# Kernel optimization log

Hardware: AMD Instinct MI355X
Metric: run time of the kernel (lower is better)

Reference implementation:

```python
import jax, jax.numpy as jnp
import numpy as np

B, S, D, H, L = 32, 512, 512, 8, 6
NQ, FF, V, C = 8, 2048, 32000, 10
DK = D // H
EPS = 1e-5


def _layernorm(x, g, b):
    mu = jnp.mean(x, axis=-1, keepdims=True)
    var = jnp.mean(jnp.square(x - mu), axis=-1, keepdims=True)
    return (x - mu) * jax.lax.rsqrt(var + EPS) * g + b


def _pos_encoding(seq_len, dim):
    pos = jnp.arange(seq_len, dtype=jnp.float32)[:, None]
    div = jnp.exp(jnp.arange(0, dim, 2, dtype=jnp.float32) * (-jnp.log(10000.0) / dim))
    pe = jnp.zeros((seq_len, dim), dtype=jnp.float32)
    pe = pe.at[:, 0::2].set(jnp.sin(pos * div))
    pe = pe.at[:, 1::2].set(jnp.cos(pos * div))
    return pe


def setup_inputs() -> dict:
    key = jax.random.key(0)
    ks = jax.random.split(key, 16)
    sd = 0.02
    return {
        "x": jax.random.randint(ks[0], (B, S), 0, V),
        "emb": jax.random.normal(ks[1], (V, D), jnp.float32) * sd,
        "ln1_g": jnp.ones((L, D), jnp.float32),
        "ln1_b": jnp.zeros((L, D), jnp.float32),
        "ln2_g": jnp.ones((L, D), jnp.float32),
        "ln2_b": jnp.zeros((L, D), jnp.float32),
        "attn_w": jax.random.normal(ks[2], (L, D, D), jnp.float32) * sd,
        "attn_b": jnp.zeros((L, D), jnp.float32),
        "theta": jax.random.normal(ks[3], (L, NQ), jnp.float32),
        "ffn_w1": jax.random.normal(ks[4], (L, NQ, FF), jnp.float32) * sd,
        "ffn_b1": jnp.zeros((L, FF), jnp.float32),
        "ffn_w2": jax.random.normal(ks[5], (L, FF, D), jnp.float32) * sd,
        "ffn_b2": jnp.zeros((L, D), jnp.float32),
        "clf_w": jax.random.normal(ks[6], (D, C), jnp.float32) * sd,
        "clf_b": jnp.zeros((C,), jnp.float32),
    }


def reference(x, emb, ln1_g, ln1_b, ln2_g, ln2_b, attn_w, attn_b, theta,
              ffn_w1, ffn_b1, ffn_w2, ffn_b2, clf_w, clf_b):
    h = emb[x] + _pos_encoding(S, D)[None]  # [B,S,D]
    scale = 1.0 / jnp.sqrt(jnp.float32(DK))
    for l in range(L):
        # --- MultiHeadAttentionQuantum: q=k=v=reshape(x), no projections ---
        q = h.reshape(B, S, H, DK)
        scores = jnp.einsum('bihd,bjhd->bhij', q, q) * scale
        p = jax.nn.softmax(scores, axis=-1)
        attn = jnp.einsum('bhij,bjhd->bihd', p, q).reshape(B, S, D)
        attn = attn @ attn_w[l] + attn_b[l]
        h = _layernorm(h + attn, ln1_g[l], ln1_b[l])
        # --- FeedForwardQuantum: per-wire RX-encode -> RY(theta) -> <Z> = cos(x)cos(theta) ---
        qout = jnp.cos(h[..., :NQ]) * jnp.cos(theta[l])  # [B,S,NQ]
        f = jax.nn.relu(qout @ ffn_w1[l] + ffn_b1[l]) @ ffn_w2[l] + ffn_b2[l]
        h = _layernorm(h + f, ln2_g[l], ln2_b[l])
    pooled = jnp.mean(h, axis=1)  # [B,D]
    return pooled @ clf_w + clf_b  # [B,C]
```

## Files before the change

### kernel.cpp

```cpp
#include <hip/hip_runtime.h>
#include <hip/hip_bf16.h>
#include <math.h>

#define BB 32
#define SS 512
#define DD 512
#define HH 8
#define DK 64
#define LL 6
#define NQ 8
#define FF 2048
#define CC 10

typedef unsigned int uint;
typedef unsigned short ushort_t;
using bf16x8 = __attribute__((ext_vector_type(8))) short;
using f32x4  = __attribute__((ext_vector_type(4))) float;

#define MFMA(a, b, c) __builtin_amdgcn_mfma_f32_16x16x32_bf16((a), (b), (c), 0, 0, 0)

union U8 { ushort_t u[8]; bf16x8 v; };

__device__ __forceinline__ void gload16(const void* g, void* l) {
    __builtin_amdgcn_global_load_lds((__attribute__((address_space(1))) void*)g,
                                     (__attribute__((address_space(3))) void*)l,
                                     16, 0, 0);
}

__device__ inline ushort_t f2bf(float x) {
    uint u = __float_as_uint(x);
    u += 0x7FFFu + ((u >> 16) & 1u);
    return (ushort_t)(u >> 16);
}
__device__ inline void tsplit(float v, ushort_t& hi, ushort_t& lo) {
    uint u = __float_as_uint(v);
    hi = (ushort_t)(u >> 16);
    lo = f2bf(v - __uint_as_float(u & 0xFFFF0000u));
}
__device__ inline void tsplit_fast(float v, ushort_t& hi, ushort_t& lo) {
    uint u = __float_as_uint(v);
    hi = (ushort_t)(u >> 16);
    float res = v - __uint_as_float(u & 0xFFFF0000u);
    lo = (ushort_t)(__float_as_uint(res) >> 16);
}
__device__ inline uint packsplit(float v) {
    uint u = __float_as_uint(v) & 0xFFFF0000u;
    uint ru = __float_as_uint(v - __uint_as_float(u));
    ru += 0x7FFFu + ((ru >> 16) & 1u);
    return u | (ru >> 16);
}
__device__ inline float unpackf(uint u) {
    return __uint_as_float(u & 0xFFFF0000u) + __uint_as_float(u << 16);
}

__global__ __launch_bounds__(256) void embed_pe(const int* __restrict__ x,
                                                const float* __restrict__ emb,
                                                uint* __restrict__ Hp) {
    int idx = blockIdx.x * 256 + threadIdx.x;
    if (idx >= BB * SS * DD) return;
    int d = idx & (DD - 1);
    int s = (idx >> 9) & (SS - 1);
    int tok = x[idx >> 9];
    int i2 = d >> 1;
    float freq = expf((float)(2 * i2) * (-9.210340371976184f / (float)DD));
    float ang = (float)s * freq;
    float pe = (d & 1) ? cosf(ang) : sinf(ang);
    Hp[idx] = packsplit(emb[(size_t)tok * DD + d] + pe);
}

__global__ __launch_bounds__(256) void transpose_split_w(const float* __restrict__ in,
                                                         ushort_t* __restrict__ outh,
                                                         ushort_t* __restrict__ outl,
                                                         int K, int N) {
    __shared__ ushort_t th[64][68], tl[64][68];
    int nb = N >> 6;
    int k0 = ((int)blockIdx.x / nb) << 6;
    int n0 = ((int)blockIdx.x % nb) << 6;
    int t = threadIdx.x;
    int r = t >> 2, cb = (t & 3) << 4;
#pragma unroll
    for (int c = 0; c < 4; c++) {
        float4 v = *reinterpret_cast<const float4*>(&in[(size_t)(k0 + r) * N + n0 + cb + 4 * c]);
        float vv[4] = {v.x, v.y, v.z, v.w};
#pragma unroll
        for (int e = 0; e < 4; e++) {
            ushort_t hb, lb; tsplit(vv[e], hb, lb);
            th[r][cb + 4 * c + e] = hb;
            tl[r][cb + 4 * c + e] = lb;
        }
    }
    __syncthreads();
    int n = t >> 2, kb = (t & 3) << 4;
#pragma unroll
    for (int c = 0; c < 4; c++) {
        ushort4 oh, ol;
        oh.x = th[kb + 4 * c + 0][n]; ol.x = tl[kb + 4 * c + 0][n];
        oh.y = th[kb + 4 * c + 1][n]; ol.y = tl[kb + 4 * c + 1][n];
        oh.z = th[kb + 4 * c + 2][n]; ol.z = tl[kb + 4 * c + 2][n];
        oh.w = th[kb + 4 * c + 3][n]; ol.w = tl[kb + 4 * c + 3][n];
        *reinterpret_cast<ushort4*>(&outh[(size_t)(n0 + n) * K + k0 + kb + 4 * c]) = oh;
        *reinterpret_cast<ushort4*>(&outl[(size_t)(n0 + n) * K + k0 + kb + 4 * c]) = ol;
    }
}

__global__ __launch_bounds__(256) void prep_w1t(const float* __restrict__ W1all,
                                                ushort_t* __restrict__ outh,
                                                ushort_t* __restrict__ outl) {
    int l = blockIdx.y;
    int f = blockIdx.x * 256 + threadIdx.x;
    const float* W1 = W1all + (size_t)l * NQ * FF;
    U8 ph, pl;
#pragma unroll
    for (int n = 0; n < 8; n++) {
        ushort_t hb, lb; tsplit(W1[n * FF + f], hb, lb);
        ph.u[n] = hb; pl.u[n] = lb;
    }
    *reinterpret_cast<bf16x8*>(&outh[((size_t)l * FF + f) * 8]) = ph.v;
    *reinterpret_cast<bf16x8*>(&outl[((size_t)l * FF + f) * 8]) = pl.v;
}

__global__ __launch_bounds__(512, 4) void flash_attn_split(const uint* __restrict__ Hp,
                                                           ushort_t* __restrict__ outh,
                                                           ushort_t* __restrict__ outl) {
    __shared__ __align__(16) ushort_t Kh[64][72], Kl[64][72];
    __shared__ __align__(16) ushort_t Vh[64][72], Vl[64][72];
    __shared__ __align__(16) ushort_t Ph[128][72], Pl[128][72];

    int i0 = blockIdx.x * 128;
    int h0 = blockIdx.y * DK;
    int b  = blockIdx.z;
    const uint* baseH = Hp + (size_t)b * (SS * DD);

    int t = threadIdx.x;
    int w = t >> 6;
    int ln = t & 63;
    int l15 = ln & 15, lh = ln >> 4;

    bf16x8 aqh0, aqh1, aql0, aql1;
    {
        int row = i0 + w * 16 + l15;
        const uint* src = &baseH[(size_t)row * DD + h0 + lh * 8];
        uint4 p0 = *reinterpret_cast<const uint4*>(src);
        uint4 p1 = *reinterpret_cast<const uint4*>(src + 4);
        uint4 p2 = *reinterpret_cast<const uint4*>(src + 32);
        uint4 p3 = *reinterpret_cast<const uint4*>(src + 36);
        uint a0[8] = {p0.x, p0.y, p0.z, p0.w, p1.x, p1.y, p1.z, p1.w};
        uint a1[8] = {p2.x, p2.y, p2.z, p2.w, p3.x, p3.y, p3.z, p3.w};
        U8 h0u, l0u, h1u, l1u;
#pragma unroll
        for (int e = 0; e < 8; e++) {
            h0u.u[e] = (ushort_t)(a0[e] >> 16);
            l0u.u[e] = (ushort_t)(a0[e] & 0xFFFFu);
            h1u.u[e] = (ushort_t)(a1[e] >> 16);
            l1u.u[e] = (ushort_t)(a1[e] & 0xFFFFu);
        }
        aqh0 = h0u.v; aql0 = l0u.v; aqh1 = h1u.v; aql1 = l1u.v;
    }

    float m_[4], l_[4], al[4];
    f32x4 acc[4];
    f32x4 z4 = {0.f, 0.f, 0.f, 0.f};
#pragma unroll
    for (int r = 0; r < 4; r++) { m_[r] = -1e30f; l_[r] = 0.f; acc[r] = z4; }

    int kr = t >> 3, kcb = (t & 7) * 8;
    int vc = t & 7, vr = t >> 3;

    for (int j0 = 0; j0 < SS; j0 += 64) {
        __syncthreads();
        {
            const uint* src = &baseH[(size_t)(j0 + kr) * DD + h0 + kcb];
            uint4 p0 = *reinterpret_cast<const uint4*>(src);
            uint4 p1 = *reinterpret_cast<const uint4*>(src + 4);
            uint a[8] = {p0.x, p0.y, p0.z, p0.w, p1.x, p1.y, p1.z, p1.w};
            U8 kh, kl;
#pragma unroll
            for (int e = 0; e < 8; e++) {
                kh.u[e] = (ushort_t)(a[e] >> 16);
                kl.u[e] = (ushort_t)(a[e] & 0xFFFFu);
            }
            *reinterpret_cast<bf16x8*>(&Kh[kr][kcb]) = kh.v;
            *reinterpret_cast<bf16x8*>(&Kl[kr][kcb]) = kl.v;
        }
        __syncthreads();
#pragma unroll
        for (int e = 0; e < 8; e++) {
            int d = vc + 8 * e;
            Vh[d][vr] = Kh[vr][d];
            Vl[d][vr] = Kl[vr][d];
        }
        f32x4 sc[4];
#pragma unroll
        for (int tt = 0; tt < 4; tt++) {
            bf16x8 bh0 = *reinterpret_cast<const bf16x8*>(&Kh[tt * 16 + l15][lh * 8]);
            bf16x8 bh1 = *reinterpret_cast<const bf16x8*>(&Kh[tt * 16 + l15][32 + lh * 8]);
            bf16x8 bl0 = *reinterpret_cast<const bf16x8*>(&Kl[tt * 16 + l15][lh * 8]);
            bf16x8 bl1 = *reinterpret_cast<const bf16x8*>(&Kl[tt * 16 + l15][32 + lh * 8]);
            f32x4 s = z4;
            s = MFMA(aqh0, bh0, s);
            s = MFMA(aqh1, bh1, s);
            s = MFMA(aqh0, bl0, s);
            s = MFMA(aqh1, bl1, s);
            s = MFMA(aql0, bh0, s);
            s = MFMA(aql1, bh1, s);
            sc[tt] = s * 0.125f;
        }
#pragma unroll
        for (int r = 0; r < 4; r++) {
            float mx = fmaxf(fmaxf(sc[0][r], sc[1][r]), fmaxf(sc[2][r], sc[3][r]));
            mx = fmaxf(mx, __shfl_xor(mx, 1));
            mx = fmaxf(mx, __shfl_xor(mx, 2));
            mx = fmaxf(mx, __shfl_xor(mx, 4));
            mx = fmaxf(mx, __shfl_xor(mx, 8));
            float nm = fmaxf(m_[r], mx);
            al[r] = __expf(m_[r] - nm);
            m_[r] = nm;
            float rs = 0.f;
#pragma unroll
            for (int tt = 0; tt < 4; tt++) {
                float p = __expf(sc[tt][r] - nm);
                sc[tt][r] = p;
                rs += p;
            }
            rs += __shfl_xor(rs, 1);
            rs += __shfl_xor(rs, 2);
            rs += __shfl_xor(rs, 4);
            rs += __shfl_xor(rs, 8);
            l_[r] = l_[r] * al[r] + rs;
        }
#pragma unroll
        for (int tt = 0; tt < 4; tt++)
#pragma unroll
            for (int r = 0; r < 4; r++) {
                ushort_t hb, lb; tsplit(sc[tt][r], hb, lb);
                Ph[w * 16 + lh * 4 + r][tt * 16 + l15] = hb;
                Pl[w * 16 + lh * 4 + r][tt * 16 + l15] = lb;
            }
        __syncthreads();
#pragma unroll
        for (int td = 0; td < 4; td++) {
            acc[td][0] *= al[0];
            acc[td][1] *= al[1];
            acc[td][2] *= al[2];
            acc[td][3] *= al[3];
        }
        bf16x8 aph0 = *reinterpret_cast<const bf16x8*>(&Ph[w * 16 + l15][lh * 8]);
        bf16x8 aph1 = *reinterpret_cast<const bf16x8*>(&Ph[w * 16 + l15][32 + lh * 8]);
        bf16x8 apl0 = *reinterpret_cast<const bf16x8*>(&Pl[w * 16 + l15][lh * 8]);
        bf16x8 apl1 = *reinterpret_cast<const bf16x8*>(&Pl[w * 16 + l15][32 + lh * 8]);
#pragma unroll
        for (int td = 0; td < 4; td++) {
            bf16x8 bvh0 = *reinterpret_cast<const bf16x8*>(&Vh[td * 16 + l15][lh * 8]);
            bf16x8 bvh1 = *reinterpret_cast<const bf16x8*>(&Vh[td * 16 + l15][32 + lh * 8]);
            bf16x8 bvl0 = *reinterpret_cast<const bf16x8*>(&Vl[td * 16 + l15][lh * 8]);
            bf16x8 bvl1 = *reinterpret_cast<const bf16x8*>(&Vl[td * 16 + l15][32 + lh * 8]);
            acc[td] = MFMA(aph0, bvh0, acc[td]);
            acc[td] = MFMA(aph1, bvh1, acc[td]);
            acc[td] = MFMA(aph0, bvl0, acc[td]);
            acc[td] = MFMA(aph1, bvl1, acc[td]);
            acc[td] = MFMA(apl0, bvh0, acc[td]);
            acc[td] = MFMA(apl1, bvh1, acc[td]);
        }
    }

#pragma unroll
    for (int r = 0; r < 4; r++) {
        float inv = 1.f / l_[r];
        int row = i0 + w * 16 + lh * 4 + r;
#pragma unroll
        for (int td = 0; td < 4; td++) {
            float o = acc[td][r] * inv;
            ushort_t hb, lb; tsplit(o, hb, lb);
            size_t idx = (size_t)b * SS * DD + (size_t)row * DD + h0 + td * 16 + l15;
            outh[idx] = hb;
            outl[idx] = lb;
        }
    }
}

#define SWZREAD(plane, row, ks) \
    (*reinterpret_cast<const bf16x8*>(&(plane)[row][((((ks) * 4 + lh) ^ ((row) & 7)) * 8)]))

__global__ __launch_bounds__(512, 4) void gemm_split(const ushort_t* __restrict__ Ah,
                                                     const ushort_t* __restrict__ Al,
                                                     const ushort_t* __restrict__ Bth,
                                                     const ushort_t* __restrict__ Btl,
                                                     const float* __restrict__ bias,
                                                     float* __restrict__ C,
                                                     int M, int N, int K) {
    __shared__ __align__(16) ushort_t sAh[128][64], sAl[128][64];
    __shared__ __align__(16) ushort_t sBh[128][64], sBl[128][64];
    int nb = N >> 7;
    int m0 = ((int)blockIdx.x / nb) << 7;
    int n0 = ((int)blockIdx.x % nb) << 7;
    int t = threadIdx.x;
    int w = t >> 6, ln = t & 63, l15 = ln & 15, lh = ln >> 4;
    int wr = (w >> 2) * 64, wc = (w & 3) * 32;

    f32x4 z4 = {0.f, 0.f, 0.f, 0.f};
    f32x4 acc[4][2];
#pragma unroll
    for (int i = 0; i < 4; i++)
#pragma unroll
        for (int j = 0; j < 2; j++) acc[i][j] = z4;

    int srow = ln >> 3;
    int schunk = (ln & 7) ^ srow;

    int ntile = K >> 6;
    for (int kt = 0; kt < ntile; kt++) {
        __syncthreads();
        int kk = kt * 64;
#pragma unroll
        for (int p = 0; p < 2; p++) {
            int rbase = (w + p * 8) * 8;
            int grow = rbase + srow;
            int gc = kk + schunk * 8;
            gload16(&Ah[(size_t)(m0 + grow) * K + gc],  &sAh[rbase][0]);
            gload16(&Al[(size_t)(m0 + grow) * K + gc],  &sAl[rbase][0]);
            gload16(&Bth[(size_t)(n0 + grow) * K + gc], &sBh[rbase][0]);
            gload16(&Btl[(size_t)(n0 + grow) * K + gc], &sBl[rbase][0]);
        }
        __syncthreads();
#pragma unroll
        for (int ks = 0; ks < 2; ks++) {
            bf16x8 ah[4], al_[4];
#pragma unroll
            for (int mt = 0; mt < 4; mt++) {
                int row = wr + mt * 16 + l15;
                ah[mt]  = SWZREAD(sAh, row, ks);
                al_[mt] = SWZREAD(sAl, row, ks);
            }
#pragma unroll
            for (int nt = 0; nt < 2; nt++) {
                int row = wc + nt * 16 + l15;
                bf16x8 bh = SWZREAD(sBh, row, ks);
                bf16x8 bl = SWZREAD(sBl, row, ks);
#pragma unroll
                for (int mt = 0; mt < 4; mt++) {
                    acc[mt][nt] = MFMA(ah[mt], bh, acc[mt][nt]);
                    acc[mt][nt] = MFMA(ah[mt], bl, acc[mt][nt]);
                    acc[mt][nt] = MFMA(al_[mt], bh, acc[mt][nt]);
                }
            }
        }
    }
#pragma unroll
    for (int nt = 0; nt < 2; nt++) {
        int col = n0 + wc + nt * 16 + l15;
        float bs = bias[col];
#pragma unroll
        for (int mt = 0; mt < 4; mt++)
#pragma unroll
            for (int r = 0; r < 4; r++)
                C[(size_t)(m0 + wr + mt * 16 + lh * 4 + r) * N + col] = acc[mt][nt][r] + bs;
    }
}

__global__ __launch_bounds__(256) void ln_residual(uint* __restrict__ Hp,
                                                   const float* __restrict__ add,
                                                   const float* __restrict__ g,
                                                   const float* __restrict__ bta) {
    int row = blockIdx.x * 4 + (threadIdx.x >> 6);
    int lane = threadIdx.x & 63;
    uint* hp = Hp + (size_t)row * DD;
    const float* ap = add + (size_t)row * DD;
    float v[8];
    float sum = 0.f;
#pragma unroll
    for (int i = 0; i < 8; i++) {
        int d = lane + i * 64;
        v[i] = unpackf(hp[d]) + ap[d];
        sum += v[i];
    }
#pragma unroll
    for (int off = 32; off > 0; off >>= 1) sum += __shfl_xor(sum, off);
    float mu = sum * (1.f / DD);
    float s2 = 0.f;
#pragma unroll
    for (int i = 0; i < 8; i++) {
        float d2 = v[i] - mu;
        s2 += d2 * d2;
    }
#pragma unroll
    for (int off = 32; off > 0; off >>= 1) s2 += __shfl_xor(s2, off);
    float inv = rsqrtf(s2 * (1.f / DD) + 1e-5f);
#pragma unroll
    for (int i = 0; i < 8; i++) {
        int d = lane + i * 64;
        hp[d] = packsplit((v[i] - mu) * inv * g[d] + bta[d]);
    }
}

__global__ __launch_bounds__(512, 4) void ffn_split(const uint* __restrict__ Hp,
                                                    const ushort_t* __restrict__ W1th,
                                                    const ushort_t* __restrict__ W1tl,
                                                    const float* __restrict__ b1,
                                                    const ushort_t* __restrict__ W2th,
                                                    const ushort_t* __restrict__ W2tl,
                                                    const float* __restrict__ b2,
                                                    const float* __restrict__ theta,
                                                    float* __restrict__ outp) {
    __shared__ __align__(16) ushort_t Abh[128][72], Abl[128][72];
    __shared__ __align__(16) ushort_t sBh[128][64], sBl[128][64];
    __shared__ __align__(16) ushort_t qsh[129][8], qsl[129][8];
    __shared__ float tcs[8];

    int t = threadIdx.x;
    int m0 = (int)(blockIdx.x >> 2) * 128;
    int n0 = (int)(blockIdx.x & 3) * 128;
    if (t < 8) {
        tcs[t] = cosf(theta[t]);
        qsh[128][t] = 0;
        qsl[128][t] = 0;
    }
    __syncthreads();
#pragma unroll
    for (int i = 0; i < 2; i++) {
        int idx = t + i * 512;
        int m = idx >> 3, n = idx & 7;
        float q = cosf(unpackf(Hp[(size_t)(m0 + m) * DD + n])) * tcs[n];
        ushort_t hb, lb; tsplit(q, hb, lb);
        qsh[m][n] = hb;
        qsl[m][n] = lb;
    }

    int w = t >> 6, ln = t & 63, l15 = ln & 15, lh = ln >> 4;
    int wr = (w >> 2) * 64, wc = (w & 3) * 32;
    bool lh0 = (lh == 0);
    f32x4 z4 = {0.f, 0.f, 0.f, 0.f};
    bf16x8 z8 = {0, 0, 0, 0, 0, 0, 0, 0};
    f32x4 acc[4][2];
#pragma unroll
    for (int i = 0; i < 4; i++)
#pragma unroll
        for (int j = 0; j < 2; j++) acc[i][j] = z4;

    int srow = ln >> 3;
    int schunk = (ln & 7) ^ srow;

    bf16x8 rwh[4], rwl[4];
#pragma unroll
    for (int fq = 0; fq < 4; fq++) {
        rwh[fq] = *reinterpret_cast<const bf16x8*>(&W1th[(size_t)(fq * 16 + l15) * 8]);
        rwl[fq] = *reinterpret_cast<const bf16x8*>(&W1tl[(size_t)(fq * 16 + l15) * 8]);
    }

    for (int k0 = 0; k0 < FF; k0 += 64) {
        __syncthreads();
#pragma unroll
        for (int p = 0; p < 2; p++) {
            int rbase = (w + p * 8) * 8;
            int grow = rbase + srow;
            int gc = k0 + schunk * 8;
            gload16(&W2th[(size_t)(n0 + grow) * FF + gc], &sBh[rbase][0]);
            gload16(&W2tl[(size_t)(n0 + grow) * FF + gc], &sBl[rbase][0]);
        }
        {
            bf16x8 wh[4], wl[4];
#pragma unroll
            for (int fq = 0; fq < 4; fq++) {
                wh[fq] = lh0 ? rwh[fq] : z8;
                wl[fq] = lh0 ? rwl[fq] : z8;
            }
            int m = w * 16 + l15;
            int mrow = lh0 ? m : 128;
            bf16x8 qh  = *reinterpret_cast<const bf16x8*>(&qsh[mrow][0]);
            bf16x8 ql_ = *reinterpret_cast<const bf16x8*>(&qsl[mrow][0]);
#pragma unroll
            for (int fq = 0; fq < 4; fq++) {
                f32x4 d = z4;
                d = MFMA(wh[fq], qh, d);
                d = MFMA(wh[fq], ql_, d);
                d = MFMA(wl[fq], qh, d);
                float4 b1v = *reinterpret_cast<const float4*>(&b1[k0 + fq * 16 + lh * 4]);
                float v0 = fmaxf(d[0] + b1v.x, 0.f);
                float v1 = fmaxf(d[1] + b1v.y, 0.f);
                float v2 = fmaxf(d[2] + b1v.z, 0.f);
                float v3 = fmaxf(d[3] + b1v.w, 0.f);
                ushort_t h0_, l0_, h1_, l1_, h2_, l2_, h3_, l3_;
                tsplit_fast(v0, h0_, l0_);
                tsplit_fast(v1, h1_, l1_);
                tsplit_fast(v2, h2_, l2_);
                tsplit_fast(v3, h3_, l3_);
                uint2 hu, lu;
                hu.x = (uint)h0_ | ((uint)h1_ << 16);
                hu.y = (uint)h2_ | ((uint)h3_ << 16);
                lu.x = (uint)l0_ | ((uint)l1_ << 16);
                lu.y = (uint)l2_ | ((uint)l3_ << 16);
                *reinterpret_cast<uint2*>(&Abh[m][fq * 16 + lh * 4]) = hu;
                *reinterpret_cast<uint2*>(&Abl[m][fq * 16 + lh * 4]) = lu;
            }
        }
        __syncthreads();
        if (k0 + 64 < FF) {
            int k1 = k0 + 64;
#pragma unroll
            for (int fq = 0; fq < 4; fq++) {
                rwh[fq] = *reinterpret_cast<const bf16x8*>(&W1th[(size_t)(k1 + fq * 16 + l15) * 8]);
                rwl[fq] = *reinterpret_cast<const bf16x8*>(&W1tl[(size_t)(k1 + fq * 16 + l15) * 8]);
            }
        }
#pragma unroll
        for (int ks = 0; ks < 2; ks++) {
            bf16x8 ah[4], al_[4];
#pragma unroll
            for (int mt = 0; mt < 4; mt++) {
                ah[mt]  = *reinterpret_cast<const bf16x8*>(&Abh[wr + mt * 16 + l15][ks * 32 + lh * 8]);
                al_[mt] = *reinterpret_cast<const bf16x8*>(&Abl[wr + mt * 16 + l15][ks * 32 + lh * 8]);
            }
#pragma unroll
            for (int nt = 0; nt < 2; nt++) {
                int row = wc + nt * 16 + l15;
                bf16x8 bh = SWZREAD(sBh, row, ks);
                bf16x8 bl = SWZREAD(sBl, row, ks);
#pragma unroll
                for (int mt = 0; mt < 4; mt++) {
                    acc[mt][nt] = MFMA(ah[mt], bh, acc[mt][nt]);
                    acc[mt][nt] = MFMA(ah[mt], bl, acc[mt][nt]);
                    acc[mt][nt] = MFMA(al_[mt], bh, acc[mt][nt]);
                }
            }
        }
    }
#pragma unroll
    for (int nt = 0; nt < 2; nt++) {
        int col = n0 + wc + nt * 16 + l15;
        float bs = b2[col];
#pragma unroll
        for (int mt = 0; mt < 4; mt++)
#pragma unroll
            for (int r = 0; r < 4; r++)
                outp[(size_t)(m0 + wr + mt * 16 + lh * 4 + r) * DD + col] = acc[mt][nt][r] + bs;
    }
}

__global__ __launch_bounds__(256) void pool_mean(const uint* __restrict__ Hp,
                                                 float* __restrict__ pooled) {
    int idx = blockIdx.x * 256 + threadIdx.x;
    if (idx >= BB * DD) return;
    int b = idx >> 9, d = idx & 511;
    float s = 0.f;
    for (int j = 0; j < SS; j++) s += unpackf(Hp[((size_t)b * SS + j) * DD + d]);
    pooled[idx] = s * (1.f / SS);
}

__global__ __launch_bounds__(64) void classifier(const float* __restrict__ pooled,
                                                 const float* __restrict__ W,
                                                 const float* __restrict__ bias,
                                                 float* __restrict__ out) {
    int o = blockIdx.x;
    int b = o / CC, c = o % CC;
    int lane = threadIdx.x;
    float s = 0.f;
    for (int d = lane; d < DD; d += 64) s += pooled[b * DD + d] * W[d * CC + c];
#pragma unroll
    for (int off = 32; off > 0; off >>= 1) s += __shfl_xor(s, off);
    if (lane == 0) out[o] = s + bias[c];
}

extern "C" void kernel_launch(void* const* d_in, const int* in_sizes, int n_in,
                              void* d_out, int out_size, void* d_ws, size_t ws_size,
                              hipStream_t stream) {
    (void)in_sizes; (void)n_in; (void)out_size; (void)ws_size;
    const int*   x      = (const int*)d_in[0];
    const float* emb    = (const float*)d_in[1];
    const float* ln1_g  = (const float*)d_in[2];
    const float* ln1_b  = (const float*)d_in[3];
    const float* ln2_g  = (const float*)d_in[4];
    const float* ln2_b  = (const float*)d_in[5];
    const float* attn_w = (const float*)d_in[6];
    const float* attn_b = (const float*)d_in[7];
    const float* theta  = (const float*)d_in[8];
    const float* ffn_w1 = (const float*)d_in[9];
    const float* ffn_b1 = (const float*)d_in[10];
    const float* ffn_w2 = (const float*)d_in[11];
    const float* ffn_b2 = (const float*)d_in[12];
    const float* clf_w  = (const float*)d_in[13];
    const float* clf_b  = (const float*)d_in[14];
    float* out = (float*)d_out;

    char* ws = (char*)d_ws;
    uint*     Hp     = (uint*)(ws);
    float*    t2     = (float*)(ws + 33554432);
    ushort_t* t1h    = (ushort_t*)(ws + 67108864);
    ushort_t* t1l    = (ushort_t*)(ws + 83886080);
    float*    pooled = (float*)(ws + 100663296);
    ushort_t* Wath   = (ushort_t*)(ws + 100728832);
    ushort_t* Watl   = (ushort_t*)(ws + 101253120);
    ushort_t* W1th6  = (ushort_t*)(ws + 101777408);
    ushort_t* W1tl6  = (ushort_t*)(ws + 101974016);
    ushort_t* W2th   = (ushort_t*)(ws + 67108864);
    ushort_t* W2tl   = (ushort_t*)(ws + 67108864 + 2097152);

    embed_pe<<<(BB * SS * DD + 255) / 256, 256, 0, stream>>>(x, emb, Hp);
    prep_w1t<<<dim3(FF / 256, LL), 256, 0, stream>>>(ffn_w1, W1th6, W1tl6);

    for (int l = 0; l < LL; l++) {
        flash_attn_split<<<dim3(SS / 128, HH, BB), 512, 0, stream>>>(Hp, t1h, t1l);
        transpose_split_w<<<(DD / 64) * (DD / 64), 256, 0, stream>>>(
            attn_w + (size_t)l * DD * DD, Wath, Watl, DD, DD);
        gemm_split<<<(16384 / 128) * (DD / 128), 512, 0, stream>>>(
            t1h, t1l, Wath, Watl, attn_b + l * DD, t2, BB * SS, DD, DD);
        ln_residual<<<BB * SS / 4, 256, 0, stream>>>(Hp, t2, ln1_g + l * DD, ln1_b + l * DD);
        transpose_split_w<<<(FF / 64) * (DD / 64), 256, 0, stream>>>(
            ffn_w2 + (size_t)l * FF * DD, W2th, W2tl, FF, DD);
        ffn_split<<<(16384 / 128) * (DD / 128), 512, 0, stream>>>(
            Hp, W1th6 + (size_t)l * FF * 8, W1tl6 + (size_t)l * FF * 8, ffn_b1 + l * FF,
            W2th, W2tl, ffn_b2 + l * DD, theta + l * NQ, t2);
        ln_residual<<<BB * SS / 4, 256, 0, stream>>>(Hp, t2, ln2_g + l * DD, ln2_b + l * DD);
    }

    pool_mean<<<(BB * DD + 255) / 256, 256, 0, stream>>>(Hp, pooled);
    classifier<<<BB * CC, 64, 0, stream>>>(pooled, clf_w, clf_b, out);
}
```

Before: 1.941 ms.

## Rework attention output GEMM to 256 threads with 64x64 warp tiles

The split-bf16 attention projection GEMM drops from 512 to 256 threads per block, so each wave now computes a 64x64 output tile instead of 64x32. The aim is to reuse each loaded A fragment across more MFMAs and to cut the number of LDS reads per MFMA. The async global_load_lds path with XOR swizzle is replaced by plain register-staged uint4 copies into LDS rows padded to 72 elements, which avoids bank conflicts without swizzling. The trade-off is higher register pressure, fewer waves to hide latency, and loss of the direct-to-LDS loads.

New measurement: 1.851 ms. -4.6%, faster.

```diff
diff --git a/kernel.cpp b/kernel.cpp
--- a/kernel.cpp
+++ b/kernel.cpp
@@ -278,48 +278,44 @@
     }
 }
 
-#define SWZREAD(plane, row, ks) \
-    (*reinterpret_cast<const bf16x8*>(&(plane)[row][((((ks) * 4 + lh) ^ ((row) & 7)) * 8)]))
-
-__global__ __launch_bounds__(512, 4) void gemm_split(const ushort_t* __restrict__ Ah,
+__global__ __launch_bounds__(256, 2) void gemm_split(const ushort_t* __restrict__ Ah,
                                                      const ushort_t* __restrict__ Al,
                                                      const ushort_t* __restrict__ Bth,
                                                      const ushort_t* __restrict__ Btl,
                                                      const float* __restrict__ bias,
                                                      float* __restrict__ C,
                                                      int M, int N, int K) {
-    __shared__ __align__(16) ushort_t sAh[128][64], sAl[128][64];
-    __shared__ __align__(16) ushort_t sBh[128][64], sBl[128][64];
+    __shared__ __align__(16) ushort_t Abh[128][72], Abl[128][72];
+    __shared__ __align__(16) ushort_t Bbh[128][72], Bbl[128][72];
     int nb = N >> 7;
     int m0 = ((int)blockIdx.x / nb) << 7;
     int n0 = ((int)blockIdx.x % nb) << 7;
     int t = threadIdx.x;
     int w = t >> 6, ln = t & 63, l15 = ln & 15, lh = ln >> 4;
-    int wr = (w >> 2) * 64, wc = (w & 3) * 32;
+    int wr = (w >> 1) * 64, wc = (w & 1) * 64;
 
     f32x4 z4 = {0.f, 0.f, 0.f, 0.f};
-    f32x4 acc[4][2];
+    f32x4 acc[4][4];
 #pragma unroll
     for (int i = 0; i < 4; i++)
 #pragma unroll
-        for (int j = 0; j < 2; j++) acc[i][j] = z4;
-
-    int srow = ln >> 3;
-    int schunk = (ln & 7) ^ srow;
-
-    int ntile = K >> 6;
-    for (int kt = 0; kt < ntile; kt++) {
+        for (int j = 0; j < 4; j++) acc[i][j] = z4;
+
+    int arr = t >> 3, akk = (t & 7) * 8;
+
+    for (int k0 = 0; k0 < K; k0 += 64) {
         __syncthreads();
-        int kk = kt * 64;
-#pragma unroll
-        for (int p = 0; p < 2; p++) {
-            int rbase = (w + p * 8) * 8;
-            int grow = rbase + srow;
-            int gc = kk + schunk * 8;
-            gload16(&Ah[(size_t)(m0 + grow) * K + gc],  &sAh[rbase][0]);
-            gload16(&Al[(size_t)(m0 + grow) * K + gc],  &sAl[rbase][0]);
-            gload16(&Bth[(size_t)(n0 + grow) * K + gc], &sBh[rbase][0]);
-            gload16(&Btl[(size_t)(n0 + grow) * K + gc], &sBl[rbase][0]);
+#pragma unroll
+        for (int r = 0; r < 4; r++) {
+            int row = arr + r * 32;
+            *reinterpret_cast<uint4*>(&Abh[row][akk]) =
+                *reinterpret_cast<const uint4*>(&Ah[(size_t)(m0 + row) * K + k0 + akk]);
+            *reinterpret_cast<uint4*>(&Abl[row][akk]) =
+                *reinterpret_cast<const uint4*>(&Al[(size_t)(m0 + row) * K + k0 + akk]);
+            *reinterpret_cast<uint4*>(&Bbh[row][akk]) =
+                *reinterpret_cast<const uint4*>(&Bth[(size_t)(n0 + row) * K + k0 + akk]);
+            *reinterpret_cast<uint4*>(&Bbl[row][akk]) =
+                *reinterpret_cast<const uint4*>(&Btl[(size_t)(n0 + row) * K + k0 + akk]);
         }
         __syncthreads();
 #pragma unroll
@@ -327,15 +323,13 @@
             bf16x8 ah[4], al_[4];
 #pragma unroll
             for (int mt = 0; mt < 4; mt++) {
-                int row = wr + mt * 16 + l15;
-                ah[mt]  = SWZREAD(sAh, row, ks);
-                al_[mt] = SWZREAD(sAl, row, ks);
-            }
-#pragma unroll
-            for (int nt = 0; nt < 2; nt++) {
-                int row = wc + nt * 16 + l15;
-                bf16x8 bh = SWZREAD(sBh, row, ks);
-                bf16x8 bl = SWZREAD(sBl, row, ks);
+                ah[mt]  = *reinterpret_cast<const bf16x8*>(&Abh[wr + mt * 16 + l15][ks * 32 + lh * 8]);
+                al_[mt] = *reinterpret_cast<const bf16x8*>(&Abl[wr + mt * 16 + l15][ks * 32 + lh * 8]);
+            }
+#pragma unroll
+            for (int nt = 0; nt < 4; nt++) {
+                bf16x8 bh = *reinterpret_cast<const bf16x8*>(&Bbh[wc + nt * 16 + l15][ks * 32 + lh * 8]);
+                bf16x8 bl = *reinterpret_cast<const bf16x8*>(&Bbl[wc + nt * 16 + l15][ks * 32 + lh * 8]);
 #pragma unroll
                 for (int mt = 0; mt < 4; mt++) {
                     acc[mt][nt] = MFMA(ah[mt], bh, acc[mt][nt]);
@@ -346,7 +340,7 @@
         }
     }
 #pragma unroll
-    for (int nt = 0; nt < 2; nt++) {
+    for (int nt = 0; nt < 4; nt++) {
         int col = n0 + wc + nt * 16 + l15;
         float bs = bias[col];
 #pragma unroll
@@ -391,6 +385,9 @@
         hp[d] = packsplit((v[i] - mu) * inv * g[d] + bta[d]);
     }
 }
+
+#define SWZREAD(plane, row, ks) \
+    (*reinterpret_cast<const bf16x8*>(&(plane)[row][((((ks) * 4 + lh) ^ ((row) & 7)) * 8)]))
 
 __global__ __launch_bounds__(512, 4) void ffn_split(const uint* __restrict__ Hp,
                                                     const ushort_t* __restrict__ W1th,
@@ -600,7 +597,7 @@
         flash_attn_split<<<dim3(SS / 128, HH, BB), 512, 0, stream>>>(Hp, t1h, t1l);
         transpose_split_w<<<(DD / 64) * (DD / 64), 256, 0, stream>>>(
             attn_w + (size_t)l * DD * DD, Wath, Watl, DD, DD);
-        gemm_split<<<(16384 / 128) * (DD / 128), 512, 0, stream>>>(
+        gemm_split<<<(16384 / 128) * (DD / 128), 256, 0, stream>>>(
             t1h, t1l, Wath, Watl, attn_b + l * DD, t2, BB * SS, DD, DD);
         ln_residual<<<BB * SS / 4, 256, 0, stream>>>(Hp, t2, ln1_g + l * DD, ln1_b + l * DD);
         transpose_split_w<<<(FF / 64) * (DD / 64), 256, 0, stream>>>(
```
